# Optimization experiments

Measured on AMD Instinct MI355X. Metric: run time of the kernel, lower is better.

Reference implementation:

```python
import jax, jax.numpy as jnp
import numpy as np

HEADS = 16

def setup_inputs() -> dict:
    key = jax.random.key(0)
    k0, k1, k2, k3 = jax.random.split(key, 4)
    B, L, D = 2, 2048, 2048
    q = jax.random.normal(k0, (B, L, D), dtype=jnp.float32)
    k = jax.random.normal(k1, (B, L, D), dtype=jnp.float32)
    v = jax.random.normal(k2, (B, L, D), dtype=jnp.float32)
    wo = jax.random.normal(k3, (D, D), dtype=jnp.float32) * (1.0 / np.sqrt(D))
    return {"q": q, "k": k, "v": v, "wo": wo}

def reference(q, k, v, wo):
    B, Lq, D = q.shape
    Lk = k.shape[1]
    H = HEADS
    hd = D // H
    # [B, L, D] -> [B, H, L, hd]
    qh = q.reshape(B, Lq, H, hd).transpose(0, 2, 1, 3)
    kh = k.reshape(B, Lk, H, hd).transpose(0, 2, 1, 3)
    vh = v.reshape(B, Lk, H, hd).transpose(0, 2, 1, 3)
    scale = 1.0 / np.sqrt(hd).astype(np.float32)
    scores = jnp.einsum('bhqd,bhkd->bhqk', qh, kh) * scale
    cache_len = Lk - Lq
    # additive causal mask: -10000 above diagonal offset cache_len+1
    mask = jnp.triu(jnp.full((Lq, Lk), -10000.0, dtype=scores.dtype), k=cache_len + 1)
    attn = jax.nn.softmax(scores + mask, axis=-1)  # dropout p=0.0 => identity
    out = jnp.einsum('bhqk,bhkd->bhqd', attn, vh)
    out = out.transpose(0, 2, 1, 3).reshape(B, Lq, D)
    out = out @ wo.T  # torch Linear: x @ W^T
    return (out, kh, vh)
```

## Files before the change

kernel.cpp:

```cpp
#include <hip/hip_runtime.h>


typedef __attribute__((ext_vector_type(8))) __bf16 bf16x8;
typedef __attribute__((ext_vector_type(4))) float f32x4;

__device__ __forceinline__ unsigned short f2bf(float f) {
  union { float f; unsigned int u; } v; v.f = f;
  return (unsigned short)((v.u + 0x7FFFu + ((v.u >> 16) & 1u)) >> 16);
}
__device__ __forceinline__ __bf16 tobf(float f) {
  unsigned short u = f2bf(f);
  __bf16 r;
  __builtin_memcpy(&r, &u, 2);
  return r;
}
__device__ __forceinline__ f32x4 zero4() {
  f32x4 z = {0.0f, 0.0f, 0.0f, 0.0f};
  return z;
}
__device__ __forceinline__ void gld_lds16(const unsigned short* g, unsigned short* l) {
  __builtin_amdgcn_global_load_lds(
      (const __attribute__((address_space(1))) unsigned int*)g,
      (__attribute__((address_space(3))) unsigned int*)l, 16, 0, 0);
}

__global__ __launch_bounds__(256) void conv_k(const float* __restrict__ k,
                                              float* __restrict__ kh,
                                              unsigned short* __restrict__ kbf) {
  int t = blockIdx.x * 256 + threadIdx.x;
  int d4 = t & 31;
  int l  = (t >> 5) & 2047;
  int h  = (t >> 16) & 15;
  int b  = t >> 20;
  const float4 v = *(const float4*)(k + ((size_t)(b * 2048 + l)) * 2048 + h * 128 + d4 * 4);
  size_t dst = (size_t)t * 4;
  *(float4*)(kh + dst) = v;
  *(ushort4*)(kbf + dst) = make_ushort4(f2bf(v.x), f2bf(v.y), f2bf(v.z), f2bf(v.w));
}

__global__ __launch_bounds__(256) void conv_wo(const float* __restrict__ wo,
                                               unsigned short* __restrict__ wobf) {
  int t = blockIdx.x * 256 + threadIdx.x;
  size_t dst = (size_t)t * 4;
  const float4 v = *(const float4*)(wo + dst);
  *(ushort4*)(wobf + dst) = make_ushort4(f2bf(v.x), f2bf(v.y), f2bf(v.z), f2bf(v.w));
}

__global__ __launch_bounds__(256) void conv_v(const float* __restrict__ v,
                                              float* __restrict__ vh,
                                              unsigned short* __restrict__ vbt) {
  __shared__ __align__(16) unsigned short T[128 * 72];
  const int tid = threadIdx.x;
  const int bid = blockIdx.x;
  const int lt = bid & 31;
  const int h  = (bid >> 5) & 15;
  const int b  = bid >> 9;
  const int l0 = lt * 64;
  const int bh = b * 16 + h;
#pragma unroll
  for (int i = 0; i < 8; ++i) {
    int c = tid + 256 * i;
    int row = c >> 5, col4 = c & 31;
    const float4 x = *(const float4*)(v + ((size_t)(b * 2048 + l0 + row)) * 2048 + h * 128 + col4 * 4);
    *(float4*)(vh + ((size_t)(bh * 2048 + l0 + row)) * 128 + col4 * 4) = x;
    T[(col4 * 4 + 0) * 72 + row] = f2bf(x.x);
    T[(col4 * 4 + 1) * 72 + row] = f2bf(x.y);
    T[(col4 * 4 + 2) * 72 + row] = f2bf(x.z);
    T[(col4 * 4 + 3) * 72 + row] = f2bf(x.w);
  }
  __syncthreads();
#pragma unroll
  for (int i = 0; i < 4; ++i) {
    int c = tid + 256 * i;
    int dR = c >> 3, colL = (c & 7) * 8;
    *(uint4*)(vbt + ((size_t)(bh * 128 + dR)) * 2048 + l0 + colL) = *(const uint4*)&T[dR * 72 + colL];
  }
}

__global__ __launch_bounds__(256) void flash_attn(const float* __restrict__ q,
                                                  const unsigned short* __restrict__ kbf,
                                                  const unsigned short* __restrict__ vbt,
                                                  unsigned short* __restrict__ ctx) {
  __shared__ __align__(16) unsigned short K2[2][64 * 128];
  __shared__ __align__(16) unsigned short V2[2][128 * 64];
  __shared__ __align__(16) unsigned short Pl[4][16 * 76];
  __shared__ float Lw[4][16];
  const int tid = threadIdx.x;
  const int w = tid >> 6, lane = tid & 63;
  const int lo = lane & 15, quad = lane >> 4;
  const int bid = blockIdx.x;
  const int pair = bid & 15;
  const int bh = bid >> 4;
  const int b = bh >> 4, h = bh & 15;
  const unsigned short* kg0 = kbf + (size_t)bh * 2048 * 128;
  const unsigned short* vg0 = vbt + (size_t)bh * 128 * 2048;
  const float qscale = 0.08838834764831845f * 1.4426950408889634f;

  auto stage = [&](int buf, int k0) {
#pragma unroll
    for (int i = 0; i < 4; ++i) {
      int c = tid + 256 * i;
      int row = c >> 4, p = c & 15;
      int g = (p & 8) | ((p & 7) ^ (row & 7));
      gld_lds16(kg0 + (size_t)(k0 + row) * 128 + g * 8, &K2[buf][(w * 64 + 256 * i) * 8]);
    }
#pragma unroll
    for (int i = 0; i < 4; ++i) {
      int c = tid + 256 * i;
      int row = c >> 3, p = c & 7;
      int g = p ^ (row & 7);
      gld_lds16(vg0 + (size_t)row * 2048 + k0 + g * 8, &V2[buf][(w * 64 + 256 * i) * 8]);
    }
  };

  for (int phase = 0; phase < 2; ++phase) {
    const int qt = phase ? 31 - pair : pair;
    const int q0 = qt * 64;

    stage(0, 0);

    bf16x8 qf[4];
    {
      const float* qb = q + ((size_t)(b * 2048 + q0 + w * 16 + lo)) * 2048 + h * 128;
#pragma unroll
      for (int kb = 0; kb < 4; ++kb) {
        float4 x = *(const float4*)(qb + kb * 32 + quad * 8);
        float4 y = *(const float4*)(qb + kb * 32 + quad * 8 + 4);
        bf16x8 f;
        f[0] = tobf(x.x * qscale); f[1] = tobf(x.y * qscale);
        f[2] = tobf(x.z * qscale); f[3] = tobf(x.w * qscale);
        f[4] = tobf(y.x * qscale); f[5] = tobf(y.y * qscale);
        f[6] = tobf(y.z * qscale); f[7] = tobf(y.w * qscale);
        qf[kb] = f;
      }
    }

    f32x4 o[8];
#pragma unroll
    for (int i = 0; i < 8; ++i) o[i] = zero4();
    float lsum[4] = {0.f, 0.f, 0.f, 0.f};

    for (int kt = 0; kt <= qt; ++kt) {
      __syncthreads();
      if (kt < qt) stage((kt + 1) & 1, (kt + 1) * 64);
      const int buf = kt & 1;
      const int k0 = kt * 64;

      f32x4 s[4];
#pragma unroll
      for (int nb = 0; nb < 4; ++nb) {
        f32x4 z = zero4();
#pragma unroll
        for (int kb = 0; kb < 4; ++kb) {
          int row = nb * 16 + lo;
          int g = kb * 4 + quad;
          int p = (g & 8) | ((g & 7) ^ (row & 7));
          bf16x8 kf = *(const bf16x8*)&K2[buf][row * 128 + p * 8];
          z = __builtin_amdgcn_mfma_f32_16x16x32_bf16(qf[kb], kf, z, 0, 0, 0);
        }
        s[nb] = z;
      }

      if (kt == qt) {
#pragma unroll
        for (int nb = 0; nb < 4; ++nb) {
          int key = k0 + nb * 16 + lo;
#pragma unroll
          for (int r = 0; r < 4; ++r) {
            int rowA = q0 + w * 16 + quad * 4 + r;
            if (key > rowA) s[nb][r] = -1e30f;
          }
        }
      }

      unsigned short* pw = &Pl[w][0];
#pragma unroll
      for (int nb = 0; nb < 4; ++nb)
#pragma unroll
        for (int r = 0; r < 4; ++r) {
          float p = __builtin_amdgcn_exp2f(s[nb][r]);
          unsigned int u = __builtin_bit_cast(unsigned int, p);
          lsum[r] += __builtin_bit_cast(float, u & 0xffff0000u);
          pw[(quad * 4 + r) * 76 + nb * 16 + lo] = (unsigned short)(u >> 16);
        }
      __asm__ volatile("s_waitcnt lgkmcnt(0)" ::: "memory");

#pragma unroll
      for (int ob = 0; ob < 8; ++ob) {
#pragma unroll
        for (int kb2 = 0; kb2 < 2; ++kb2) {
          bf16x8 pa = *(const bf16x8*)&pw[lo * 76 + kb2 * 32 + quad * 8];
          int row = ob * 16 + lo;
          int g = kb2 * 4 + quad;
          int p = g ^ (row & 7);
          bf16x8 vf = *(const bf16x8*)&V2[buf][row * 64 + p * 8];
          o[ob] = __builtin_amdgcn_mfma_f32_16x16x32_bf16(vf, pa, o[ob], 0, 0, 0);
        }
      }
    }
    __syncthreads();

#pragma unroll
    for (int r = 0; r < 4; ++r) {
      lsum[r] += __shfl_xor(lsum[r], 1);
      lsum[r] += __shfl_xor(lsum[r], 2);
      lsum[r] += __shfl_xor(lsum[r], 4);
      lsum[r] += __shfl_xor(lsum[r], 8);
    }
    if (lo == 0) {
#pragma unroll
      for (int r = 0; r < 4; ++r) Lw[w][quad * 4 + r] = lsum[r];
    }
    __asm__ volatile("s_waitcnt lgkmcnt(0)" ::: "memory");
    const float linv = 1.0f / Lw[w][lo];

    unsigned short* cb = ctx + ((size_t)(b * 2048 + q0 + w * 16 + lo)) * 2048 + h * 128 + quad * 4;
#pragma unroll
    for (int ob = 0; ob < 8; ++ob) {
      ushort4 pk = make_ushort4(f2bf(o[ob][0] * linv), f2bf(o[ob][1] * linv),
                                f2bf(o[ob][2] * linv), f2bf(o[ob][3] * linv));
      *(ushort4*)(cb + ob * 16) = pk;
    }
  }
}

__global__ __launch_bounds__(256) void gemm_bt(const unsigned short* __restrict__ A,
                                               const unsigned short* __restrict__ Bm,
                                               float* __restrict__ C) {
  __shared__ __align__(16) unsigned short As[2][128 * 64];
  __shared__ __align__(16) unsigned short Bs[2][128 * 64];
  const int tid = threadIdx.x;
  const int w = tid >> 6, lane = tid & 63;
  const int lo = lane & 15, quad = lane >> 4;
  const int nbid = blockIdx.x & 15;
  const int mbid = blockIdx.x >> 4;
  const int m0 = mbid * 128, n0 = nbid * 128;
  const int wr = w >> 1, wc = w & 1;

  auto stage = [&](int buf, int k0) {
#pragma unroll
    for (int i = 0; i < 4; ++i) {
      int c = tid + 256 * i;
      int row = c >> 3, p = c & 7;
      int g = p ^ (row & 7);
      gld_lds16(A + (size_t)(m0 + row) * 2048 + k0 + g * 8, &As[buf][(w * 64 + 256 * i) * 8]);
    }
#pragma unroll
    for (int i = 0; i < 4; ++i) {
      int c = tid + 256 * i;
      int row = c >> 3, p = c & 7;
      int g = p ^ (row & 7);
      gld_lds16(Bm + (size_t)(n0 + row) * 2048 + k0 + g * 8, &Bs[buf][(w * 64 + 256 * i) * 8]);
    }
  };

  f32x4 acc[4][4];
#pragma unroll
  for (int i = 0; i < 4; ++i)
#pragma unroll
    for (int j = 0; j < 4; ++j) acc[i][j] = zero4();

  stage(0, 0);
  for (int kt = 0; kt < 32; ++kt) {
    __syncthreads();
    if (kt < 31) stage((kt + 1) & 1, (kt + 1) * 64);
    const int buf = kt & 1;
#pragma unroll
    for (int kb = 0; kb < 2; ++kb) {
      bf16x8 af[4], bfr[4];
#pragma unroll
      for (int mi = 0; mi < 4; ++mi) {
        int row = wr * 64 + mi * 16 + lo;
        int g = kb * 4 + quad;
        int p = g ^ (row & 7);
        af[mi] = *(const bf16x8*)&As[buf][row * 64 + p * 8];
      }
#pragma unroll
      for (int ni = 0; ni < 4; ++ni) {
        int row = wc * 64 + ni * 16 + lo;
        int g = kb * 4 + quad;
        int p = g ^ (row & 7);
        bfr[ni] = *(const bf16x8*)&Bs[buf][row * 64 + p * 8];
      }
#pragma unroll
      for (int mi = 0; mi < 4; ++mi)
#pragma unroll
        for (int ni = 0; ni < 4; ++ni)
          acc[mi][ni] = __builtin_amdgcn_mfma_f32_16x16x32_bf16(af[mi], bfr[ni], acc[mi][ni], 0, 0, 0);
    }
  }
#pragma unroll
  for (int mi = 0; mi < 4; ++mi)
#pragma unroll
    for (int ni = 0; ni < 4; ++ni)
#pragma unroll
      for (int r = 0; r < 4; ++r) {
        int row = m0 + wr * 64 + mi * 16 + quad * 4 + r;
        int col = n0 + wc * 64 + ni * 16 + lo;
        C[(size_t)row * 2048 + col] = acc[mi][ni][r];
      }
}

extern "C" void kernel_launch(void* const* d_in, const int* in_sizes, int n_in,
                              void* d_out, int out_size, void* d_ws, size_t ws_size,
                              hipStream_t stream) {
  const float* q  = (const float*)d_in[0];
  const float* k  = (const float*)d_in[1];
  const float* v  = (const float*)d_in[2];
  const float* wo = (const float*)d_in[3];

  float* outp = (float*)d_out;
  float* kh   = outp + 8388608;
  float* vh   = outp + 16777216;

  unsigned short* ws   = (unsigned short*)d_ws;
  unsigned short* kbf  = ws;
  unsigned short* vbt  = kbf + 8388608;
  unsigned short* wobf = vbt + 8388608;
  unsigned short* ctx  = wobf + 4194304;

  conv_k<<<8192, 256, 0, stream>>>(k, kh, kbf);
  conv_v<<<1024, 256, 0, stream>>>(v, vh, vbt);
  conv_wo<<<4096, 256, 0, stream>>>(wo, wobf);
  flash_attn<<<512, 256, 0, stream>>>(q, kbf, vbt, ctx);
  gemm_bt<<<512, 256, 0, stream>>>(ctx, wobf, outp);
}
```

Baseline: 318.3 us.

## Keep attention probabilities in registers by transposing QK MFMA and permuting V layout

Swaps the operand order of the QK^T MFMA so each lane holds scores for one query row across keys. Packed bf16 probabilities then feed the PV MFMA directly from registers, with no round trip through the per-warp LDS P buffer. The V transpose kernel writes keys in a permuted order within each 16-key group so the register-held P matches the V operand layout. The row-sum reduction shrinks to two cross-lane shuffles, and the LDS scratch for P and the row sums is gone. Probabilities now use round-to-nearest bf16 instead of truncation, which changes numerics slightly.

```diff
diff --git a/kernel.cpp b/kernel.cpp
--- a/kernel.cpp
+++ b/kernel.cpp
@@ -3,6 +3,7 @@
 
 typedef __attribute__((ext_vector_type(8))) __bf16 bf16x8;
 typedef __attribute__((ext_vector_type(4))) float f32x4;
+typedef __attribute__((ext_vector_type(4))) unsigned int uint32x4;
 
 __device__ __forceinline__ unsigned short f2bf(float f) {
   union { float f; unsigned int u; } v; v.f = f;
@@ -13,6 +14,9 @@
   __bf16 r;
   __builtin_memcpy(&r, &u, 2);
   return r;
+}
+__device__ __forceinline__ float bfval(unsigned short u) {
+  return __builtin_bit_cast(float, ((unsigned int)u) << 16);
 }
 __device__ __forceinline__ f32x4 zero4() {
   f32x4 z = {0.0f, 0.0f, 0.0f, 0.0f};
@@ -72,8 +76,15 @@
 #pragma unroll
   for (int i = 0; i < 4; ++i) {
     int c = tid + 256 * i;
-    int dR = c >> 3, colL = (c & 7) * 8;
-    *(uint4*)(vbt + ((size_t)(bh * 128 + dR)) * 2048 + l0 + colL) = *(const uint4*)&T[dR * 72 + colL];
+    int dR = c >> 3, cIdx = c & 7;
+    int s2 = cIdx >> 2, qd = cIdx & 3;
+    const unsigned short* Tr = &T[dR * 72];
+    uint4 o4;
+    o4.x = *(const unsigned int*)&Tr[0 * 16 + qd * 4 + 2 * s2];
+    o4.y = *(const unsigned int*)&Tr[1 * 16 + qd * 4 + 2 * s2];
+    o4.z = *(const unsigned int*)&Tr[2 * 16 + qd * 4 + 2 * s2];
+    o4.w = *(const unsigned int*)&Tr[3 * 16 + qd * 4 + 2 * s2];
+    *(uint4*)(vbt + ((size_t)(bh * 128 + dR)) * 2048 + l0 + cIdx * 8) = o4;
   }
 }
 
@@ -83,8 +94,6 @@
                                                   unsigned short* __restrict__ ctx) {
   __shared__ __align__(16) unsigned short K2[2][64 * 128];
   __shared__ __align__(16) unsigned short V2[2][128 * 64];
-  __shared__ __align__(16) unsigned short Pl[4][16 * 76];
-  __shared__ float Lw[4][16];
   const int tid = threadIdx.x;
   const int w = tid >> 6, lane = tid & 63;
   const int lo = lane & 15, quad = lane >> 4;
@@ -116,6 +125,7 @@
   for (int phase = 0; phase < 2; ++phase) {
     const int qt = phase ? 31 - pair : pair;
     const int q0 = qt * 64;
+    const int qrow = q0 + w * 16 + lo;
 
     stage(0, 0);
 
@@ -138,7 +148,7 @@
     f32x4 o[8];
 #pragma unroll
     for (int i = 0; i < 8; ++i) o[i] = zero4();
-    float lsum[4] = {0.f, 0.f, 0.f, 0.f};
+    float lsum = 0.0f;
 
     for (int kt = 0; kt <= qt; ++kt) {
       __syncthreads();
@@ -156,7 +166,7 @@
           int g = kb * 4 + quad;
           int p = (g & 8) | ((g & 7) ^ (row & 7));
           bf16x8 kf = *(const bf16x8*)&K2[buf][row * 128 + p * 8];
-          z = __builtin_amdgcn_mfma_f32_16x16x32_bf16(qf[kb], kf, z, 0, 0, 0);
+          z = __builtin_amdgcn_mfma_f32_16x16x32_bf16(kf, qf[kb], z, 0, 0, 0);
         }
         s[nb] = z;
       }
@@ -164,62 +174,61 @@
       if (kt == qt) {
 #pragma unroll
         for (int nb = 0; nb < 4; ++nb) {
-          int key = k0 + nb * 16 + lo;
+          int keyb = k0 + nb * 16 + quad * 4;
 #pragma unroll
           for (int r = 0; r < 4; ++r) {
-            int rowA = q0 + w * 16 + quad * 4 + r;
-            if (key > rowA) s[nb][r] = -1e30f;
+            if (keyb + r > qrow) s[nb][r] = -1e30f;
           }
         }
       }
 
-      unsigned short* pw = &Pl[w][0];
-#pragma unroll
-      for (int nb = 0; nb < 4; ++nb)
-#pragma unroll
-        for (int r = 0; r < 4; ++r) {
-          float p = __builtin_amdgcn_exp2f(s[nb][r]);
-          unsigned int u = __builtin_bit_cast(unsigned int, p);
-          lsum[r] += __builtin_bit_cast(float, u & 0xffff0000u);
-          pw[(quad * 4 + r) * 76 + nb * 16 + lo] = (unsigned short)(u >> 16);
+      unsigned int pk[4][2];
+#pragma unroll
+      for (int nb = 0; nb < 4; ++nb) {
+#pragma unroll
+        for (int s2 = 0; s2 < 2; ++s2) {
+          float p0 = __builtin_amdgcn_exp2f(s[nb][2 * s2]);
+          float p1 = __builtin_amdgcn_exp2f(s[nb][2 * s2 + 1]);
+          unsigned short u0 = f2bf(p0);
+          unsigned short u1 = f2bf(p1);
+          pk[nb][s2] = (unsigned int)u0 | ((unsigned int)u1 << 16);
+          lsum += bfval(u0);
+          lsum += bfval(u1);
         }
-      __asm__ volatile("s_waitcnt lgkmcnt(0)" ::: "memory");
+      }
+
+      bf16x8 pa[2];
+#pragma unroll
+      for (int kb2 = 0; kb2 < 2; ++kb2) {
+        uint32x4 t;
+        t[0] = pk[0][kb2]; t[1] = pk[1][kb2]; t[2] = pk[2][kb2]; t[3] = pk[3][kb2];
+        pa[kb2] = __builtin_bit_cast(bf16x8, t);
+      }
 
 #pragma unroll
       for (int ob = 0; ob < 8; ++ob) {
 #pragma unroll
         for (int kb2 = 0; kb2 < 2; ++kb2) {
-          bf16x8 pa = *(const bf16x8*)&pw[lo * 76 + kb2 * 32 + quad * 8];
           int row = ob * 16 + lo;
           int g = kb2 * 4 + quad;
           int p = g ^ (row & 7);
           bf16x8 vf = *(const bf16x8*)&V2[buf][row * 64 + p * 8];
-          o[ob] = __builtin_amdgcn_mfma_f32_16x16x32_bf16(vf, pa, o[ob], 0, 0, 0);
+          o[ob] = __builtin_amdgcn_mfma_f32_16x16x32_bf16(vf, pa[kb2], o[ob], 0, 0, 0);
         }
       }
     }
     __syncthreads();
 
-#pragma unroll
-    for (int r = 0; r < 4; ++r) {
-      lsum[r] += __shfl_xor(lsum[r], 1);
-      lsum[r] += __shfl_xor(lsum[r], 2);
-      lsum[r] += __shfl_xor(lsum[r], 4);
-      lsum[r] += __shfl_xor(lsum[r], 8);
-    }
-    if (lo == 0) {
-#pragma unroll
-      for (int r = 0; r < 4; ++r) Lw[w][quad * 4 + r] = lsum[r];
-    }
-    __asm__ volatile("s_waitcnt lgkmcnt(0)" ::: "memory");
-    const float linv = 1.0f / Lw[w][lo];
+    lsum += __shfl_xor(lsum, 16);
+    lsum += __shfl_xor(lsum, 32);
+    const float linv = 1.0f / lsum;
 
     unsigned short* cb = ctx + ((size_t)(b * 2048 + q0 + w * 16 + lo)) * 2048 + h * 128 + quad * 4;
 #pragma unroll
     for (int ob = 0; ob < 8; ++ob) {
-      ushort4 pk = make_ushort4(f2bf(o[ob][0] * linv), f2bf(o[ob][1] * linv),
-                                f2bf(o[ob][2] * linv), f2bf(o[ob][3] * linv));
-      *(ushort4*)(cb + ob * 16) = pk;
+      ushort4 pkk = make_ushort4(f2bf(o[ob][0] * linv), f2bf(o[ob][1] * linv),
+                                 f2bf(o[ob][2] * linv), f2bf(o[ob][3] * linv));
+      *(ushort4*)(cb + ob * 16) = pkk;
     }
   }
 }
```

Result: no change. 316.2 us (-0.7%).
